# Performance work log

Measured on AMD Instinct MI355X. Metric: run time of the kernel, lower is better.

Reference implementation:

```python
import jax, jax.numpy as jnp
import numpy as np

N_NODES = 50000
N_EDGES = 800000
N_FEAT = 128
D_HID = 128
N_CLASS = 40


def gcn_conv(x, W, b, src, dst, n_nodes):
    """PyG GCNConv: h = D^{-1/2} (A + I) D^{-1/2} (x @ W) + b.
    src/dst are int arrays [E]; self-loops handled analytically."""
    h = x @ W  # [N, D]
    ones = jnp.ones(src.shape[0], dtype=h.dtype)
    # degree after adding self-loops: 1 + in-degree (edge weights are 1)
    deg = 1.0 + jax.ops.segment_sum(ones, dst, num_segments=n_nodes)
    dinv = jax.lax.rsqrt(deg)  # [N]
    # messages along edges src -> dst with symmetric normalization
    msg = h[src] * (dinv[src] * dinv[dst])[:, None]  # [E, D]
    agg = jax.ops.segment_sum(msg, dst, num_segments=n_nodes)  # [N, D]
    # self-loop contribution: dinv[i]^2 * h[i]
    agg = agg + h * (dinv * dinv)[:, None]
    return agg + b


def setup_inputs() -> dict:
    key = jax.random.key(0)
    ks = jax.random.split(key, 5)
    x = jax.random.normal(ks[0], (N_NODES, N_FEAT), dtype=jnp.float32)
    edge_index = jax.random.randint(ks[1], (2, N_EDGES), 0, N_NODES, dtype=jnp.int64)
    s_in = 1.0 / np.sqrt(N_FEAT)
    s_h = 1.0 / np.sqrt(D_HID)
    W_in = jax.random.normal(ks[2], (N_FEAT, D_HID), dtype=jnp.float32) * s_in
    W1 = jax.random.normal(ks[3], (D_HID, D_HID), dtype=jnp.float32) * s_h
    W_out = jax.random.normal(ks[4], (D_HID, N_CLASS), dtype=jnp.float32) * s_h
    return {
        "x": x,
        "edge_index": edge_index,
        "W_in": W_in,
        "b_in": jnp.zeros((D_HID,), jnp.float32),
        "W1": W1,
        "b1": jnp.zeros((D_HID,), jnp.float32),
        "W_out": W_out,
        "b_out": jnp.zeros((N_CLASS,), jnp.float32),
    }


def reference(x, edge_index, W_in, b_in, W1, b1, W_out, b_out):
    src, dst = edge_index[0], edge_index[1]
    n = x.shape[0]
    # input GCNConv (no activation on input_fc, matching the torch forward)
    h = gcn_conv(x, W_in, b_in, src, dst, n)
    # hidden layer: dropout is identity at eval; relu after conv; normalize=False
    h = jax.nn.relu(gcn_conv(h, W1, b1, src, dst, n))
    out = h @ W_out + b_out
    return jax.nn.log_softmax(out, axis=1)
```

## Files before the change

kernel.cpp:

```cpp
#include <hip/hip_runtime.h>
#include <math.h>


#define THREADS 256

__device__ __forceinline__ float b2f(unsigned int lo16) {
    return __uint_as_float(lo16 << 16);
}
__device__ __forceinline__ unsigned short f2b(float f) {
    unsigned int u = __float_as_uint(f);
    u += 0x7FFFu + ((u >> 16) & 1u);
    return (unsigned short)(u >> 16);
}

__global__ void detect_idx64(const int* __restrict__ idx, int* __restrict__ flag) {
    int t = threadIdx.x;
    unsigned long long b = __ballot(idx[2 * t + 1] == 0);
    if (t == 0) *flag = (b == 0xFFFFFFFFFFFFFFFFull) ? 1 : 0;
}

__global__ void fill_pos(const int* __restrict__ idx, const int* __restrict__ flag,
                         int* __restrict__ cnt, unsigned int* __restrict__ rec, int E) {
    int e = blockIdx.x * blockDim.x + threadIdx.x;
    if (e >= E) return;
    int f = *flag;
    int src, dst;
    if (f) { src = idx[2 * e]; dst = idx[2 * (E + e)]; }
    else   { src = idx[e];     dst = idx[E + e]; }
    unsigned int pos = (unsigned int)atomicAdd(&cnt[dst], 1);
    rec[e] = ((unsigned int)src << 16) | (pos & 0xFFFFu);
}

__global__ __launch_bounds__(256) void scanA(const int* __restrict__ cnt,
                                             int* __restrict__ bsum, int N) {
    __shared__ int wt[4];
    int tid = threadIdx.x, lane = tid & 63, w = tid >> 6;
    int i = blockIdx.x * 256 + tid;
    int v = (i < N) ? cnt[i] : 0;
    int s = v;
#pragma unroll
    for (int off = 1; off < 64; off <<= 1) {
        int t = __shfl_up(s, off);
        if (lane >= off) s += t;
    }
    if (lane == 63) wt[w] = s;
    __syncthreads();
    if (tid == 0) bsum[blockIdx.x] = wt[0] + wt[1] + wt[2] + wt[3];
}

__global__ __launch_bounds__(256) void scanB(int* __restrict__ bsum,
                                             int* __restrict__ boff,
                                             int* __restrict__ rowstart,
                                             int nb, int N) {
    __shared__ int wt[4];
    __shared__ int wo[5];
    int tid = threadIdx.x, lane = tid & 63, w = tid >> 6;
    int v = (tid < nb) ? bsum[tid] : 0;
    int s = v;
#pragma unroll
    for (int off = 1; off < 64; off <<= 1) {
        int t = __shfl_up(s, off);
        if (lane >= off) s += t;
    }
    if (lane == 63) wt[w] = s;
    __syncthreads();
    if (tid == 0) {
        int run = 0;
#pragma unroll
        for (int k = 0; k < 4; ++k) { wo[k] = run; run += wt[k]; }
        wo[4] = run;
    }
    __syncthreads();
    if (tid < nb) boff[tid] = wo[w] + s - v;
    if (tid == 0) rowstart[N] = wo[4];
}

__global__ __launch_bounds__(256) void scanC(const int* __restrict__ cnt,
                                             const int* __restrict__ boff,
                                             int* __restrict__ rowstart,
                                             float* __restrict__ dinv, int N) {
    __shared__ int wt[4];
    __shared__ int wo[4];
    int tid = threadIdx.x, lane = tid & 63, w = tid >> 6;
    int i = blockIdx.x * 256 + tid;
    int v = (i < N) ? cnt[i] : 0;
    int s = v;
#pragma unroll
    for (int off = 1; off < 64; off <<= 1) {
        int t = __shfl_up(s, off);
        if (lane >= off) s += t;
    }
    if (lane == 63) wt[w] = s;
    __syncthreads();
    if (tid == 0) {
        int run = 0;
#pragma unroll
        for (int k = 0; k < 4; ++k) { wo[k] = run; run += wt[k]; }
    }
    __syncthreads();
    if (i < N) {
        rowstart[i] = boff[blockIdx.x] + wo[w] + (s - v);
        dinv[i] = rsqrtf(1.0f + (float)v);
    }
}

__global__ void fill_place(const int* __restrict__ idx, const int* __restrict__ flag,
                           const unsigned int* __restrict__ rec,
                           const int* __restrict__ rowstart,
                           unsigned short* __restrict__ srcs, int E) {
    int e = blockIdx.x * blockDim.x + threadIdx.x;
    if (e >= E) return;
    int f = *flag;
    int dst = f ? idx[2 * (E + e)] : idx[E + e];
    unsigned int r = rec[e];
    srcs[rowstart[dst] + (int)(r & 0xFFFFu)] = (unsigned short)(r >> 16);
}

template <int ABF>
__global__ __launch_bounds__(256) void gemm_t(const void* __restrict__ Ap,
                                              const float* __restrict__ W,
                                              unsigned short* __restrict__ outb,
                                              int N) {
    __shared__ float Xt[128 * 64];
    __shared__ unsigned short Wl[128 * 128];
    int tid = threadIdx.x;
    int row0 = blockIdx.x * 64;

    const float4* W4 = (const float4*)W;
    ushort4* Wl4 = (ushort4*)Wl;
#pragma unroll
    for (int it = 0; it < 16; ++it) {
        int i = tid + 256 * it;
        float4 v = W4[i];
        ushort4 o;
        o.x = f2b(v.x); o.y = f2b(v.y); o.z = f2b(v.z); o.w = f2b(v.w);
        Wl4[i] = o;
    }

    {
        int r = tid >> 2, kq = tid & 3;
        int gr = row0 + r;
#pragma unroll
        for (int i = 0; i < 8; ++i) {
            int k = kq * 32 + i * 4;
            float f0, f1, f2, f3;
            if (gr < N) {
                if (ABF) {
                    uint2 qv = ((const uint2*)Ap)[(size_t)gr * 32 + (k >> 2)];
                    f0 = b2f(qv.x & 0xFFFFu); f1 = b2f(qv.x >> 16);
                    f2 = b2f(qv.y & 0xFFFFu); f3 = b2f(qv.y >> 16);
                } else {
                    float4 v = ((const float4*)Ap)[(size_t)gr * 32 + (k >> 2)];
                    f0 = v.x; f1 = v.y; f2 = v.z; f3 = v.w;
                }
            } else {
                f0 = f1 = f2 = f3 = 0.f;
            }
            Xt[(k + 0) * 64 + r] = f0;
            Xt[(k + 1) * 64 + r] = f1;
            Xt[(k + 2) * 64 + r] = f2;
            Xt[(k + 3) * 64 + r] = f3;
        }
    }
    __syncthreads();

    int cg = tid & 15;
    int rg = tid >> 4;
    float acc[4][8];
#pragma unroll
    for (int j = 0; j < 4; ++j)
#pragma unroll
        for (int c = 0; c < 8; ++c) acc[j][c] = 0.f;

    const float4* Xt4 = (const float4*)Xt;
    const uint2* Wlu = (const uint2*)Wl;
#pragma unroll 4
    for (int k = 0; k < 128; ++k) {
        float4 xv = Xt4[k * 16 + rg];
        uint2 wa = Wlu[k * 32 + cg];
        uint2 wb = Wlu[k * 32 + 16 + cg];
        float ws[8];
        ws[0] = b2f(wa.x & 0xFFFFu); ws[1] = b2f(wa.x >> 16);
        ws[2] = b2f(wa.y & 0xFFFFu); ws[3] = b2f(wa.y >> 16);
        ws[4] = b2f(wb.x & 0xFFFFu); ws[5] = b2f(wb.x >> 16);
        ws[6] = b2f(wb.y & 0xFFFFu); ws[7] = b2f(wb.y >> 16);
        float xs[4] = {xv.x, xv.y, xv.z, xv.w};
#pragma unroll
        for (int j = 0; j < 4; ++j)
#pragma unroll
            for (int c = 0; c < 8; ++c) acc[j][c] += xs[j] * ws[c];
    }

    ushort4* out4 = (ushort4*)outb;
#pragma unroll
    for (int j = 0; j < 4; ++j) {
        int r = row0 + rg * 4 + j;
        if (r < N) {
            ushort4 oa, ob;
            oa.x = f2b(acc[j][0]); oa.y = f2b(acc[j][1]);
            oa.z = f2b(acc[j][2]); oa.w = f2b(acc[j][3]);
            ob.x = f2b(acc[j][4]); ob.y = f2b(acc[j][5]);
            ob.z = f2b(acc[j][6]); ob.w = f2b(acc[j][7]);
            out4[(size_t)r * 32 + cg] = oa;
            out4[(size_t)r * 32 + 16 + cg] = ob;
        }
    }
}

__global__ __launch_bounds__(256) void agg_node(const unsigned short* __restrict__ hb,
                                                const int* __restrict__ rowstart,
                                                const unsigned short* __restrict__ srcs,
                                                const float* __restrict__ dinv,
                                                const float* __restrict__ b,
                                                unsigned short* __restrict__ outb,
                                                int N, int do_relu) {
    int w = threadIdx.x >> 6, lane = threadIdx.x & 63;
    int node = blockIdx.x * 4 + w;
    if (node >= N) return;
    int beg = rowstart[node], end = rowstart[node + 1];
    float dn = dinv[node];
    int quarter = lane >> 4, q = lane & 15;
    const uint4* hb8 = (const uint4*)hb;
    float a0 = 0.f, a1 = 0.f, a2 = 0.f, a3 = 0.f;
    float a4 = 0.f, a5 = 0.f, a6 = 0.f, a7 = 0.f;

    for (int j0 = beg; j0 < end; j0 += 64) {
        int myj = j0 + lane;
        int ms = 0;
        float md = 0.f;
        if (myj < end) { ms = (int)srcs[myj]; md = dinv[ms]; }
        int m = min(64, end - j0);
#pragma unroll 2
        for (int k = 0; k < m; k += 4) {
            int idx2 = k + quarter;
            int s = __shfl(ms, idx2);
            float c = dn * __shfl(md, idx2);
            uint4 v = hb8[(size_t)s * 16 + q];
            a0 += c * b2f(v.x & 0xFFFFu);
            a1 += c * b2f(v.x >> 16);
            a2 += c * b2f(v.y & 0xFFFFu);
            a3 += c * b2f(v.y >> 16);
            a4 += c * b2f(v.z & 0xFFFFu);
            a5 += c * b2f(v.z >> 16);
            a6 += c * b2f(v.w & 0xFFFFu);
            a7 += c * b2f(v.w >> 16);
        }
    }
    a0 += __shfl_xor(a0, 32); a1 += __shfl_xor(a1, 32);
    a2 += __shfl_xor(a2, 32); a3 += __shfl_xor(a3, 32);
    a4 += __shfl_xor(a4, 32); a5 += __shfl_xor(a5, 32);
    a6 += __shfl_xor(a6, 32); a7 += __shfl_xor(a7, 32);
    a0 += __shfl_xor(a0, 16); a1 += __shfl_xor(a1, 16);
    a2 += __shfl_xor(a2, 16); a3 += __shfl_xor(a3, 16);
    a4 += __shfl_xor(a4, 16); a5 += __shfl_xor(a5, 16);
    a6 += __shfl_xor(a6, 16); a7 += __shfl_xor(a7, 16);

    if (quarter == 0) {
        uint4 sv = hb8[(size_t)node * 16 + q];
        float d2 = dn * dn;
        float4 b0 = ((const float4*)b)[2 * q];
        float4 b1 = ((const float4*)b)[2 * q + 1];
        float r0 = a0 + d2 * b2f(sv.x & 0xFFFFu) + b0.x;
        float r1 = a1 + d2 * b2f(sv.x >> 16)     + b0.y;
        float r2 = a2 + d2 * b2f(sv.y & 0xFFFFu) + b0.z;
        float r3 = a3 + d2 * b2f(sv.y >> 16)     + b0.w;
        float r4 = a4 + d2 * b2f(sv.z & 0xFFFFu) + b1.x;
        float r5 = a5 + d2 * b2f(sv.z >> 16)     + b1.y;
        float r6 = a6 + d2 * b2f(sv.w & 0xFFFFu) + b1.z;
        float r7 = a7 + d2 * b2f(sv.w >> 16)     + b1.w;
        if (do_relu) {
            r0 = fmaxf(r0, 0.f); r1 = fmaxf(r1, 0.f);
            r2 = fmaxf(r2, 0.f); r3 = fmaxf(r3, 0.f);
            r4 = fmaxf(r4, 0.f); r5 = fmaxf(r5, 0.f);
            r6 = fmaxf(r6, 0.f); r7 = fmaxf(r7, 0.f);
        }
        uint4 o;
        o.x = (unsigned int)f2b(r0) | ((unsigned int)f2b(r1) << 16);
        o.y = (unsigned int)f2b(r2) | ((unsigned int)f2b(r3) << 16);
        o.z = (unsigned int)f2b(r4) | ((unsigned int)f2b(r5) << 16);
        o.w = (unsigned int)f2b(r6) | ((unsigned int)f2b(r7) << 16);
        ((uint4*)outb)[(size_t)node * 16 + q] = o;
    }
}

__global__ __launch_bounds__(256) void out_gemm(const unsigned short* __restrict__ h2b,
                                                const float* __restrict__ Wout,
                                                const float* __restrict__ bout,
                                                float* __restrict__ out, int N) {
    __shared__ float Xt[128 * 128];
    __shared__ float Wl[128 * 40];
    __shared__ float bl[40];
    int tid = threadIdx.x;
    int row0 = blockIdx.x * 128;

    for (int i = tid; i < 128 * 40; i += 256) Wl[i] = Wout[i];
    if (tid < 40) bl[tid] = bout[tid];

    {
        int r = tid >> 1, kh = tid & 1;
        int gr = row0 + r;
#pragma unroll
        for (int i = 0; i < 16; ++i) {
            int k = kh * 64 + i * 4;
            float f0, f1, f2, f3;
            if (gr < N) {
                uint2 qv = ((const uint2*)h2b)[(size_t)gr * 32 + (k >> 2)];
                f0 = b2f(qv.x & 0xFFFFu); f1 = b2f(qv.x >> 16);
                f2 = b2f(qv.y & 0xFFFFu); f3 = b2f(qv.y >> 16);
            } else {
                f0 = f1 = f2 = f3 = 0.f;
            }
            Xt[(k + 0) * 128 + r] = f0;
            Xt[(k + 1) * 128 + r] = f1;
            Xt[(k + 2) * 128 + r] = f2;
            Xt[(k + 3) * 128 + r] = f3;
        }
    }
    __syncthreads();

    int cg = tid & 7;
    int r4 = tid >> 3;
    float bias[5];
#pragma unroll
    for (int c = 0; c < 5; ++c) bias[c] = bl[5 * cg + c];

    float acc[4][5];
#pragma unroll
    for (int j = 0; j < 4; ++j)
#pragma unroll
        for (int c = 0; c < 5; ++c) acc[j][c] = 0.f;

    const float4* Xt4 = (const float4*)Xt;
#pragma unroll 4
    for (int k = 0; k < 128; ++k) {
        float4 xv = Xt4[k * 32 + r4];
        const float* wr = &Wl[k * 40 + 5 * cg];
        float w0 = wr[0], w1 = wr[1], w2 = wr[2], w3 = wr[3], w4 = wr[4];
        float xs[4] = {xv.x, xv.y, xv.z, xv.w};
#pragma unroll
        for (int j = 0; j < 4; ++j) {
            acc[j][0] += xs[j] * w0;
            acc[j][1] += xs[j] * w1;
            acc[j][2] += xs[j] * w2;
            acc[j][3] += xs[j] * w3;
            acc[j][4] += xs[j] * w4;
        }
    }

#pragma unroll
    for (int j = 0; j < 4; ++j) {
        int r = row0 + r4 * 4 + j;
        if (r >= N) continue;
        float v[5];
        float m = -INFINITY;
#pragma unroll
        for (int c = 0; c < 5; ++c) { v[c] = acc[j][c] + bias[c]; m = fmaxf(m, v[c]); }
        m = fmaxf(m, __shfl_xor(m, 1));
        m = fmaxf(m, __shfl_xor(m, 2));
        m = fmaxf(m, __shfl_xor(m, 4));
        float s = 0.f;
#pragma unroll
        for (int c = 0; c < 5; ++c) s += expf(v[c] - m);
        s += __shfl_xor(s, 1);
        s += __shfl_xor(s, 2);
        s += __shfl_xor(s, 4);
        float ls = logf(s);
#pragma unroll
        for (int c = 0; c < 5; ++c) out[(size_t)r * 40 + 5 * cg + c] = v[c] - m - ls;
    }
}

static inline size_t al256(size_t x) { return (x + 255) & ~(size_t)255; }

extern "C" void kernel_launch(void* const* d_in, const int* in_sizes, int n_in,
                              void* d_out, int out_size, void* d_ws, size_t ws_size,
                              hipStream_t stream) {
    const float* x     = (const float*)d_in[0];
    const int*   idx   = (const int*)d_in[1];
    const float* W_in  = (const float*)d_in[2];
    const float* b_in  = (const float*)d_in[3];
    const float* W1    = (const float*)d_in[4];
    const float* b1    = (const float*)d_in[5];
    const float* W_out = (const float*)d_in[6];
    const float* b_out = (const float*)d_in[7];
    float* out = (float*)d_out;

    int N = in_sizes[0] / 128;
    int E = in_sizes[1] / 2;

    char* ws = (char*)d_ws;
    size_t off = 0;
    int* flag = (int*)(ws + off);              off += 256;
    int* cnt = (int*)(ws + off);               off += al256((size_t)N * 4);
    int* rowstart = (int*)(ws + off);          off += al256((size_t)(N + 1) * 4);
    float* dinv = (float*)(ws + off);          off += al256((size_t)N * 4);
    unsigned short* srcs = (unsigned short*)(ws + off); off += al256((size_t)E * 2);
    unsigned int* rec = (unsigned int*)(ws + off);      off += al256((size_t)E * 4);
    int* bsum = (int*)(ws + off);              off += 2048;
    int* boff = (int*)(ws + off);              off += 2048;
    unsigned short* B0 = (unsigned short*)(ws + off);   off += (size_t)N * 128 * 2;
    unsigned short* B1 = (unsigned short*)(ws + off);

    int nb_e = (E + THREADS - 1) / THREADS;
    int nb_n = (N + THREADS - 1) / THREADS;
    int nb_g = (N + 63) / 64;
    int nb_o = (N + 127) / 128;
    int nb_a = (N + 3) / 4;

    detect_idx64<<<1, 64, 0, stream>>>(idx, flag);
    hipMemsetAsync(cnt, 0, (size_t)N * 4, stream);
    fill_pos<<<nb_e, THREADS, 0, stream>>>(idx, flag, cnt, rec, E);
    scanA<<<nb_n, THREADS, 0, stream>>>(cnt, bsum, N);
    scanB<<<1, THREADS, 0, stream>>>(bsum, boff, rowstart, nb_n, N);
    scanC<<<nb_n, THREADS, 0, stream>>>(cnt, boff, rowstart, dinv, N);
    fill_place<<<nb_e, THREADS, 0, stream>>>(idx, flag, rec, rowstart, srcs, E);

    gemm_t<0><<<nb_g, THREADS, 0, stream>>>(x, W_in, B0, N);
    agg_node<<<nb_a, THREADS, 0, stream>>>(B0, rowstart, srcs, dinv, b_in,
                                           B1, N, 0);
    gemm_t<1><<<nb_g, THREADS, 0, stream>>>(B1, W1, B0, N);
    agg_node<<<nb_a, THREADS, 0, stream>>>(B0, rowstart, srcs, dinv, b1,
                                           B1, N, 1);
    out_gemm<<<nb_o, THREADS, 0, stream>>>(B1, W_out, b_out, out, N);
}
```

Baseline: 306.9 us.

## Replace scalar FMA GEMMs with bf16 MFMA kernels using pre-packed weights

```diff
diff --git a/kernel.cpp b/kernel.cpp
--- a/kernel.cpp
+++ b/kernel.cpp
@@ -3,6 +3,9 @@
 
 
 #define THREADS 256
+
+typedef __attribute__((ext_vector_type(8))) short short8v;
+typedef __attribute__((ext_vector_type(4))) float float4v;
 
 __device__ __forceinline__ float b2f(unsigned int lo16) {
     return __uint_as_float(lo16 << 16);
@@ -116,93 +119,93 @@
     srcs[rowstart[dst] + (int)(r & 0xFFFFu)] = (unsigned short)(r >> 16);
 }
 
+__global__ __launch_bounds__(256) void pack_w(const float* __restrict__ W,
+                                              uint4* __restrict__ wpk) {
+    int tid = threadIdx.x;
+    for (int it = 0; it < 8; ++it) {
+        int s = it * 256 + tid;
+        int ct = s >> 8;
+        int kb = (s >> 6) & 3;
+        int l  = s & 63;
+        int col = ct * 16 + (l & 15);
+        int k0  = kb * 32 + ((l >> 4) << 3);
+        unsigned short e0 = f2b(W[(k0 + 0) * 128 + col]);
+        unsigned short e1 = f2b(W[(k0 + 1) * 128 + col]);
+        unsigned short e2 = f2b(W[(k0 + 2) * 128 + col]);
+        unsigned short e3 = f2b(W[(k0 + 3) * 128 + col]);
+        unsigned short e4 = f2b(W[(k0 + 4) * 128 + col]);
+        unsigned short e5 = f2b(W[(k0 + 5) * 128 + col]);
+        unsigned short e6 = f2b(W[(k0 + 6) * 128 + col]);
+        unsigned short e7 = f2b(W[(k0 + 7) * 128 + col]);
+        uint4 u;
+        u.x = (unsigned int)e0 | ((unsigned int)e1 << 16);
+        u.y = (unsigned int)e2 | ((unsigned int)e3 << 16);
+        u.z = (unsigned int)e4 | ((unsigned int)e5 << 16);
+        u.w = (unsigned int)e6 | ((unsigned int)e7 << 16);
+        wpk[s] = u;
+    }
+}
+
 template <int ABF>
-__global__ __launch_bounds__(256) void gemm_t(const void* __restrict__ Ap,
-                                              const float* __restrict__ W,
-                                              unsigned short* __restrict__ outb,
-                                              int N) {
-    __shared__ float Xt[128 * 64];
-    __shared__ unsigned short Wl[128 * 128];
+__global__ __launch_bounds__(256) void gemm_mfma(const void* __restrict__ Ap,
+                                                 const uint4* __restrict__ wpk,
+                                                 unsigned short* __restrict__ outb,
+                                                 int N) {
+    __shared__ unsigned short ol[64 * 128];
     int tid = threadIdx.x;
-    int row0 = blockIdx.x * 64;
-
-    const float4* W4 = (const float4*)W;
-    ushort4* Wl4 = (ushort4*)Wl;
-#pragma unroll
-    for (int it = 0; it < 16; ++it) {
-        int i = tid + 256 * it;
-        float4 v = W4[i];
-        ushort4 o;
-        o.x = f2b(v.x); o.y = f2b(v.y); o.z = f2b(v.z); o.w = f2b(v.w);
-        Wl4[i] = o;
-    }
-
-    {
-        int r = tid >> 2, kq = tid & 3;
-        int gr = row0 + r;
-#pragma unroll
-        for (int i = 0; i < 8; ++i) {
-            int k = kq * 32 + i * 4;
-            float f0, f1, f2, f3;
-            if (gr < N) {
-                if (ABF) {
-                    uint2 qv = ((const uint2*)Ap)[(size_t)gr * 32 + (k >> 2)];
-                    f0 = b2f(qv.x & 0xFFFFu); f1 = b2f(qv.x >> 16);
-                    f2 = b2f(qv.y & 0xFFFFu); f3 = b2f(qv.y >> 16);
-                } else {
-                    float4 v = ((const float4*)Ap)[(size_t)gr * 32 + (k >> 2)];
-                    f0 = v.x; f1 = v.y; f2 = v.z; f3 = v.w;
-                }
-            } else {
-                f0 = f1 = f2 = f3 = 0.f;
-            }
-            Xt[(k + 0) * 64 + r] = f0;
-            Xt[(k + 1) * 64 + r] = f1;
-            Xt[(k + 2) * 64 + r] = f2;
-            Xt[(k + 3) * 64 + r] = f3;
-        }
-    }
-    __syncthreads();
-
-    int cg = tid & 15;
-    int rg = tid >> 4;
-    float acc[4][8];
-#pragma unroll
-    for (int j = 0; j < 4; ++j)
-#pragma unroll
-        for (int c = 0; c < 8; ++c) acc[j][c] = 0.f;
-
-    const float4* Xt4 = (const float4*)Xt;
-    const uint2* Wlu = (const uint2*)Wl;
-#pragma unroll 4
-    for (int k = 0; k < 128; ++k) {
-        float4 xv = Xt4[k * 16 + rg];
-        uint2 wa = Wlu[k * 32 + cg];
-        uint2 wb = Wlu[k * 32 + 16 + cg];
-        float ws[8];
-        ws[0] = b2f(wa.x & 0xFFFFu); ws[1] = b2f(wa.x >> 16);
-        ws[2] = b2f(wa.y & 0xFFFFu); ws[3] = b2f(wa.y >> 16);
-        ws[4] = b2f(wb.x & 0xFFFFu); ws[5] = b2f(wb.x >> 16);
-        ws[6] = b2f(wb.y & 0xFFFFu); ws[7] = b2f(wb.y >> 16);
-        float xs[4] = {xv.x, xv.y, xv.z, xv.w};
-#pragma unroll
-        for (int j = 0; j < 4; ++j)
-#pragma unroll
-            for (int c = 0; c < 8; ++c) acc[j][c] += xs[j] * ws[c];
-    }
-
-    ushort4* out4 = (ushort4*)outb;
-#pragma unroll
-    for (int j = 0; j < 4; ++j) {
-        int r = row0 + rg * 4 + j;
-        if (r < N) {
-            ushort4 oa, ob;
-            oa.x = f2b(acc[j][0]); oa.y = f2b(acc[j][1]);
-            oa.z = f2b(acc[j][2]); oa.w = f2b(acc[j][3]);
-            ob.x = f2b(acc[j][4]); ob.y = f2b(acc[j][5]);
-            ob.z = f2b(acc[j][6]); ob.w = f2b(acc[j][7]);
-            out4[(size_t)r * 32 + cg] = oa;
-            out4[(size_t)r * 32 + 16 + cg] = ob;
+    int w = tid >> 6, l = tid & 63;
+    int lr = l & 15, lq = l >> 4;
+    int row0 = blockIdx.x * 64 + w * 16;
+    int arow = row0 + lr;
+    int arow_c = (arow < N) ? arow : (N > 0 ? N - 1 : 0);
+
+    float4v acc[8];
+#pragma unroll
+    for (int ct = 0; ct < 8; ++ct) acc[ct] = (float4v){0.f, 0.f, 0.f, 0.f};
+
+#pragma unroll
+    for (int kb = 0; kb < 4; ++kb) {
+        short8v af;
+        if (ABF) {
+            uint4 v = *(const uint4*)((const unsigned short*)Ap + (size_t)arow_c * 128 + kb * 32 + lq * 8);
+            union { uint4 u; short8v s; } cv; cv.u = v; af = cv.s;
+        } else {
+            const float* ap = (const float*)Ap + (size_t)arow_c * 128 + kb * 32 + lq * 8;
+            float4 va = *(const float4*)ap;
+            float4 vb = *(const float4*)(ap + 4);
+            uint4 u;
+            u.x = (unsigned int)f2b(va.x) | ((unsigned int)f2b(va.y) << 16);
+            u.y = (unsigned int)f2b(va.z) | ((unsigned int)f2b(va.w) << 16);
+            u.z = (unsigned int)f2b(vb.x) | ((unsigned int)f2b(vb.y) << 16);
+            u.w = (unsigned int)f2b(vb.z) | ((unsigned int)f2b(vb.w) << 16);
+            union { uint4 uu; short8v s; } cv; cv.uu = u; af = cv.s;
+        }
+#pragma unroll
+        for (int ct = 0; ct < 8; ++ct) {
+            uint4 bv = wpk[(ct * 4 + kb) * 64 + l];
+            union { uint4 u; short8v s; } cv; cv.u = bv; short8v bf = cv.s;
+            acc[ct] = __builtin_amdgcn_mfma_f32_16x16x32_bf16(af, bf, acc[ct], 0, 0, 0);
+        }
+    }
+
+#pragma unroll
+    for (int ct = 0; ct < 8; ++ct) {
+#pragma unroll
+        for (int r = 0; r < 4; ++r) {
+            int dr = lq * 4 + r;
+            ol[(w * 16 + dr) * 128 + ct * 16 + lr] = f2b(acc[ct][r]);
+        }
+    }
+    __syncthreads();
+#pragma unroll
+    for (int it = 0; it < 4; ++it) {
+        int o = it * 4096 + tid * 16;
+        int rr = o >> 8;
+        int cb = o & 255;
+        int gr = blockIdx.x * 64 + rr;
+        if (gr < N) {
+            uint4 v = *(const uint4*)((const char*)ol + o);
+            *(uint4*)((char*)outb + (size_t)gr * 256 + cb) = v;
         }
     }
 }
@@ -398,6 +401,8 @@
     unsigned int* rec = (unsigned int*)(ws + off);      off += al256((size_t)E * 4);
     int* bsum = (int*)(ws + off);              off += 2048;
     int* boff = (int*)(ws + off);              off += 2048;
+    uint4* wpk1 = (uint4*)(ws + off);          off += 32768;
+    uint4* wpk2 = (uint4*)(ws + off);          off += 32768;
     unsigned short* B0 = (unsigned short*)(ws + off);   off += (size_t)N * 128 * 2;
     unsigned short* B1 = (unsigned short*)(ws + off);
 
@@ -409,16 +414,18 @@
 
     detect_idx64<<<1, 64, 0, stream>>>(idx, flag);
     hipMemsetAsync(cnt, 0, (size_t)N * 4, stream);
+    pack_w<<<1, THREADS, 0, stream>>>(W_in, wpk1);
+    pack_w<<<1, THREADS, 0, stream>>>(W1, wpk2);
     fill_pos<<<nb_e, THREADS, 0, stream>>>(idx, flag, cnt, rec, E);
     scanA<<<nb_n, THREADS, 0, stream>>>(cnt, bsum, N);
     scanB<<<1, THREADS, 0, stream>>>(bsum, boff, rowstart, nb_n, N);
     scanC<<<nb_n, THREADS, 0, stream>>>(cnt, boff, rowstart, dinv, N);
     fill_place<<<nb_e, THREADS, 0, stream>>>(idx, flag, rec, rowstart, srcs, E);
 
-    gemm_t<0><<<nb_g, THREADS, 0, stream>>>(x, W_in, B0, N);
+    gemm_mfma<0><<<nb_g, THREADS, 0, stream>>>(x, wpk1, B0, N);
     agg_node<<<nb_a, THREADS, 0, stream>>>(B0, rowstart, srcs, dinv, b_in,
                                            B1, N, 0);
-    gemm_t<1><<<nb_g, THREADS, 0, stream>>>(B1, W1, B0, N);
+    gemm_mfma<1><<<nb_g, THREADS, 0, stream>>>(B1, wpk2, B0, N);
     agg_node<<<nb_a, THREADS, 0, stream>>>(B0, rowstart, srcs, dinv, b1,
                                            B1, N, 1);
     out_gemm<<<nb_o, THREADS, 0, stream>>>(B1, W_out, b_out, out, N);
```

Measured after the change: 263.4 us. 1.16x faster.
